# Kernel optimization log

Hardware: AMD Instinct MI355X
Metric: run time of the kernel (lower is better)

## Reference

```python
import jax, jax.numpy as jnp
import numpy as np

NVOC = 50257
DIM = 256
HID = 256
NUM_LAYERS = 2
SEQ = 128
BATCH = 16


def setup_inputs() -> dict:
    key = jax.random.key(0)
    ks = jax.random.split(key, 16)
    u = 0.1
    inp = {
        "tokens": jax.random.randint(ks[0], (SEQ, BATCH), 0, NVOC),
        "emb": jax.random.uniform(ks[1], (NVOC, DIM), jnp.float32, -u, u),
        # gate weights are zero-initialized nn.Parameters in the original; use small
        # random values so gradients/activations are non-degenerate
        "wf": jax.random.normal(ks[2], (HID, HID), jnp.float32) * 0.05,
        "uf": jax.random.normal(ks[3], (DIM, HID), jnp.float32) * 0.05,
        "bf": jnp.zeros((HID,), jnp.float32),
        "wi": jax.random.normal(ks[4], (HID, HID), jnp.float32) * 0.05,
        "ui": jax.random.normal(ks[5], (DIM, HID), jnp.float32) * 0.05,
        "bi": jnp.zeros((HID,), jnp.float32),
        "wc": jax.random.normal(ks[6], (HID, HID), jnp.float32) * 0.05,
        "uc": jax.random.normal(ks[7], (DIM, HID), jnp.float32) * 0.05,
        "bc": jnp.zeros((HID,), jnp.float32),
        "wo": jax.random.normal(ks[8], (HID, HID), jnp.float32) * 0.05,
        "uo": jax.random.normal(ks[9], (DIM, HID), jnp.float32) * 0.05,
        "bo": jnp.zeros((HID,), jnp.float32),
        "dec_w": jax.random.uniform(ks[10], (NVOC, HID), jnp.float32, -u, u),
        "dec_b": jnp.zeros((NVOC,), jnp.float32),
    }
    return inp


def reference(tokens, emb, wf, uf, bf, wi, ui, bi, wc, uc, bc, wo, uo, bo,
              dec_w, dec_b):
    # embeddings: (T, B, D); dropout is identity (eval / p honored as 0)
    x_seq = emb[tokens]

    h0 = jnp.zeros((NUM_LAYERS, BATCH, HID), jnp.float32)
    c0 = jnp.zeros((NUM_LAYERS, BATCH, HID), jnp.float32)

    def step(carry, x_t):
        h, c = carry
        x = x_t  # (B, D)
        hs, cs = [], []
        for l in range(NUM_LAYERS):  # fixed small structural loop
            hp, cp = h[l], c[l]
            f = jax.nn.sigmoid(hp @ wf + x @ uf + bf)
            i = jax.nn.sigmoid(hp @ wi + x @ ui + bi)
            o = jax.nn.sigmoid(hp @ wo + x @ uo + bo)
            g = jnp.tanh(hp @ wc + x @ uc + bc)
            cn = f * cp + i * g
            hn = o * jnp.tanh(cn)
            hs.append(hn)
            cs.append(cn)
            x = hn  # next layer consumes this layer's hidden state
        return (jnp.stack(hs), jnp.stack(cs)), x  # emit top-layer h

    (hT, cT), h_top = jax.lax.scan(step, (h0, c0), x_seq)  # h_top: (T, B, H)
    logits = jnp.einsum('tbh,vh->tbv', h_top, dec_w) + dec_b  # (T, B, V)
    return logits, hT, cT
```

## Files before the change

kernel.cpp:

```cpp
#include <hip/hip_runtime.h>
#include <hip/hip_bf16.h>

#define NVOC 50257
#define DIM 256
#define HID 256
#define NLAYER 2
#define SEQ 128
#define BATCH 16
#define GUARD (1 << 20)
#define NCHUNK 197
#define DECBLKS (32 * NCHUNK)

typedef __bf16 bf16x8 __attribute__((ext_vector_type(8)));
typedef float f32x4 __attribute__((ext_vector_type(4)));
typedef unsigned short u16;
typedef unsigned int u32;
typedef unsigned long long u64;

#define AL64(p)   __hip_atomic_load((const u64*)(p), __ATOMIC_RELAXED, __HIP_MEMORY_SCOPE_AGENT)
#define AS32(p,v) __hip_atomic_store((u32*)(p), (v), __ATOMIC_RELAXED, __HIP_MEMORY_SCOPE_AGENT)

__device__ __forceinline__ float fsig(float z) { return 1.f / (1.f + __expf(-z)); }
__device__ __forceinline__ float ftanh(float z) {
  const float x = fminf(fmaxf(z, -15.f), 15.f);
  const float e = __expf(2.f * x);
  return (e - 1.f) / (e + 1.f);
}
__device__ __forceinline__ bf16x8 cvt8(const float4 u0, const float4 u1) {
  bf16x8 v;
  v[0] = (__bf16)u0.x; v[1] = (__bf16)u0.y; v[2] = (__bf16)u0.z; v[3] = (__bf16)u0.w;
  v[4] = (__bf16)u1.x; v[5] = (__bf16)u1.y; v[6] = (__bf16)u1.z; v[7] = (__bf16)u1.w;
  return v;
}

__global__ void zero_kernel(u32* __restrict__ flg) {
  for (int i = threadIdx.x; i < SEQ * 8; i += 256) AS32(&flg[i], 0u);
}

__global__ __launch_bounds__(256) void xu_kernel(
    const int* __restrict__ tokp, const float* __restrict__ embp,
    const float* __restrict__ uF, const float* __restrict__ uI,
    const float* __restrict__ uC, const float* __restrict__ uO,
    const float* __restrict__ bF, const float* __restrict__ bI,
    const float* __restrict__ bC, const float* __restrict__ bO,
    float* __restrict__ XU)
{
  const int tid = threadIdx.x;
  const int lane = tid & 63, wv = tid >> 6, r16 = lane & 15, kgrp = lane >> 4;
  const int m0 = blockIdx.x * 16;
  const int n0 = blockIdx.y * 256 + wv * 64;
  const float* Ug[4] = {uF, uI, uC, uO};
  const float* Bp[4] = {bF, bI, bC, bO};

  bf16x8 b[4][8];
  float bias[4];
#pragma unroll
  for (int nt = 0; nt < 4; ++nt) {
    const int n = n0 + nt * 16 + r16;
    const float* U = Ug[n >> 8];
    const int c = n & 255;
    bias[nt] = Bp[n >> 8][c];
#pragma unroll
    for (int kk = 0; kk < 8; ++kk) {
      const int kb = kk * 32 + kgrp * 8;
      bf16x8 v;
#pragma unroll
      for (int e = 0; e < 8; ++e) v[e] = (__bf16)U[(size_t)(kb + e) * HID + c];
      b[nt][kk] = v;
    }
  }

  const int tok = tokp[m0 + r16];
  const float* x = embp + (size_t)tok * DIM;
  bf16x8 a[8];
#pragma unroll
  for (int kk = 0; kk < 8; ++kk) {
    const int kb = kk * 32 + kgrp * 8;
    a[kk] = cvt8(*reinterpret_cast<const float4*>(x + kb),
                 *reinterpret_cast<const float4*>(x + kb + 4));
  }
#pragma unroll
  for (int nt = 0; nt < 4; ++nt) {
    f32x4 acc = {0.f, 0.f, 0.f, 0.f};
#pragma unroll
    for (int kk = 0; kk < 8; ++kk)
      acc = __builtin_amdgcn_mfma_f32_16x16x32_bf16(a[kk], b[nt][kk], acc, 0, 0, 0);
    const int n = n0 + nt * 16 + r16;
#pragma unroll
    for (int r = 0; r < 4; ++r)
      XU[(size_t)(m0 + kgrp * 4 + r) * 1024 + n] = acc[r] + bias[nt];
  }
}

__global__ __launch_bounds__(512, 2) void mega_kernel(
    const float* __restrict__ wF, const float* __restrict__ wI,
    const float* __restrict__ wC, const float* __restrict__ wO,
    const float* __restrict__ uF, const float* __restrict__ uI,
    const float* __restrict__ uC, const float* __restrict__ uO,
    const float* __restrict__ bF, const float* __restrict__ bI,
    const float* __restrict__ bC, const float* __restrict__ bO,
    const float* __restrict__ XU, u32* __restrict__ h0w, u32* __restrict__ h1w,
    u32* __restrict__ flg, const float* __restrict__ dw,
    const float* __restrict__ dbp, float* __restrict__ dout)
{
  const int tid  = threadIdx.x;
  const int lane = tid & 63;
  const int wv   = tid >> 6;
  const int r16  = lane & 15;
  const int kgrp = lane >> 4;
  const int bx   = blockIdx.x;

  __shared__ float gbuf[4][16][72];

  if (bx >= 8) {
    const int db = bx - 8;
    const int mb = db / NCHUNK;
    const int nb = db - mb * NCHUNK;
    const int n0 = nb * 256 + wv * 32;

    bf16x8 b[2][8];
    float bb[2];
#pragma unroll
    for (int nt = 0; nt < 2; ++nt) {
      const int v = n0 + nt * 16 + r16;
      const int vc = (v < NVOC) ? v : (NVOC - 1);
      bb[nt] = dbp[vc];
      const float* bp = dw + (size_t)vc * HID + kgrp * 8;
#pragma unroll
      for (int kk = 0; kk < 8; ++kk)
        b[nt][kk] = cvt8(*reinterpret_cast<const float4*>(bp + kk * 32),
                         *reinterpret_cast<const float4*>(bp + kk * 32 + 4));
    }

    if (tid == 0) {
      const int tl = mb * 4 + 3;
      int gd = 0;
      for (;;) {
        const u64 f0 = AL64(flg + (size_t)tl * 8 + 4);
        const u64 f1 = AL64(flg + (size_t)tl * 8 + 6);
        if (((u32)f0 & (u32)(f0 >> 32) & (u32)f1 & (u32)(f1 >> 32)) != 0u) break;
        if (++gd >= GUARD) break;
        __builtin_amdgcn_s_sleep(64);
      }
    }
    __syncthreads();

    const u16* htb = (const u16*)h1w;
    bf16x8 a[4][8];
#pragma unroll
    for (int mt = 0; mt < 4; ++mt) {
      const u16* ap = htb + ((size_t)(mb * 64 + mt * 16 + r16)) * HID + kgrp * 8;
#pragma unroll
      for (int kk = 0; kk < 8; ++kk)
        a[mt][kk] = *reinterpret_cast<const bf16x8*>(ap + kk * 32);
    }

    f32x4 acc[4][2];
#pragma unroll
    for (int mt = 0; mt < 4; ++mt)
#pragma unroll
      for (int nt = 0; nt < 2; ++nt) {
        acc[mt][nt][0] = 0.f; acc[mt][nt][1] = 0.f;
        acc[mt][nt][2] = 0.f; acc[mt][nt][3] = 0.f;
      }
#pragma unroll
    for (int kk = 0; kk < 8; ++kk)
#pragma unroll
      for (int nt = 0; nt < 2; ++nt) {
        const bf16x8 bv = b[nt][kk];
#pragma unroll
        for (int mt = 0; mt < 4; ++mt)
          acc[mt][nt] = __builtin_amdgcn_mfma_f32_16x16x32_bf16(a[mt][kk], bv, acc[mt][nt], 0, 0, 0);
      }

#pragma unroll
    for (int nt = 0; nt < 2; ++nt) {
      const int v = n0 + nt * 16 + r16;
      if (v < NVOC) {
#pragma unroll
        for (int mt = 0; mt < 4; ++mt)
#pragma unroll
          for (int r = 0; r < 4; ++r)
            dout[(size_t)(mb * 64 + mt * 16 + kgrp * 4 + r) * NVOC + v] = acc[mt][nt][r] + bb[nt];
      }
    }
    return;
  }

  const int colt = wv & 3;
  const int gp   = wv >> 2;
  const int l    = bx >> 2;
  const int jj   = bx & 3;
  const int n    = jj * 64 + colt * 16 + r16;
  const int g0   = gp * 2;

  const float* Wg[4] = {wF, wI, wC, wO};
  const float* Ug[4] = {uF, uI, uC, uO};
  const float* Bg[4] = {bF, bI, bC, bO};
  const u16* h0s = (const u16*)h0w;
  const u16* h1s = (const u16*)h1w;
  const size_t logitsN = (size_t)SEQ * BATCH * NVOC;

  bf16x8 wa[2][8];
  bf16x8 wb[2][8];
  float bias[2];
#pragma unroll
  for (int gi = 0; gi < 2; ++gi) {
    const int g = g0 + gi;
    bias[gi] = Bg[g][n];
#pragma unroll
    for (int kk = 0; kk < 8; ++kk) {
      const int kb = kk * 32 + kgrp * 8;
      bf16x8 v;
#pragma unroll
      for (int e = 0; e < 8; ++e) v[e] = (__bf16)Wg[g][(size_t)(kb + e) * HID + n];
      wa[gi][kk] = v;
      if (l == 1) {
        bf16x8 u;
#pragma unroll
        for (int e = 0; e < 8; ++e) u[e] = (__bf16)Ug[g][(size_t)(kb + e) * HID + n];
        wb[gi][kk] = u;
      }
    }
  }

  const int eb = tid >> 5;
  const int ec = (tid & 31) * 2;
  float c0 = 0.f, c1 = 0.f;

  for (int t = 0; t < SEQ; ++t) {
    f32x4 acc[2];
#pragma unroll
    for (int gi = 0; gi < 2; ++gi) { acc[gi][0]=0.f; acc[gi][1]=0.f; acc[gi][2]=0.f; acc[gi][3]=0.f; }

    float xuv[2][4];
    if (l == 0) {
#pragma unroll
      for (int gi = 0; gi < 2; ++gi)
#pragma unroll
        for (int r = 0; r < 4; ++r)
          xuv[gi][r] = XU[(size_t)(t * 16 + kgrp * 4 + r) * 1024 + (g0 + gi) * 256 + n];

      if (t > 0) {
        if (tid == 0) {
          int gd = 0;
          for (;;) {
            const u64 f0 = AL64(flg + (size_t)(t - 1) * 8);
            const u64 f1 = AL64(flg + (size_t)(t - 1) * 8 + 2);
            if (((u32)f0 & (u32)(f0 >> 32) & (u32)f1 & (u32)(f1 >> 32)) != 0u) break;
            if (++gd >= GUARD) break;
          }
        }
        __syncthreads();
        const u16* hp = h0s + ((size_t)(t - 1) * BATCH + r16) * HID + kgrp * 8;
        bf16x8 hA[8];
#pragma unroll
        for (int kk = 0; kk < 8; ++kk)
          hA[kk] = *reinterpret_cast<const bf16x8*>(hp + kk * 32);
#pragma unroll
        for (int kk = 0; kk < 8; ++kk)
#pragma unroll
          for (int gi = 0; gi < 2; ++gi)
            acc[gi] = __builtin_amdgcn_mfma_f32_16x16x32_bf16(hA[kk], wa[gi][kk], acc[gi], 0, 0, 0);
      }
    } else {
      if (t > 0) {
        if (tid == 0) {
          int gd = 0;
          for (;;) {
            const u64 g1 = AL64(flg + (size_t)(t - 1) * 8 + 4);
            const u64 g2 = AL64(flg + (size_t)(t - 1) * 8 + 6);
            if (((u32)g1 & (u32)(g1 >> 32) & (u32)g2 & (u32)(g2 >> 32)) != 0u) break;
            if (++gd >= GUARD) break;
          }
        }
        __syncthreads();
        const u16* hp = h1s + ((size_t)(t - 1) * BATCH + r16) * HID + kgrp * 8;
        bf16x8 hB[8];
#pragma unroll
        for (int kk = 0; kk < 8; ++kk)
          hB[kk] = *reinterpret_cast<const bf16x8*>(hp + kk * 32);
#pragma unroll
        for (int kk = 0; kk < 8; ++kk)
#pragma unroll
          for (int gi = 0; gi < 2; ++gi)
            acc[gi] = __builtin_amdgcn_mfma_f32_16x16x32_bf16(hB[kk], wa[gi][kk], acc[gi], 0, 0, 0);
      }
      if (tid == 0) {
        int gd = 0;
        for (;;) {
          const u64 f0 = AL64(flg + (size_t)t * 8);
          const u64 f1 = AL64(flg + (size_t)t * 8 + 2);
          if (((u32)f0 & (u32)(f0 >> 32) & (u32)f1 & (u32)(f1 >> 32)) != 0u) break;
          if (++gd >= GUARD) break;
        }
      }
      __syncthreads();
      const u16* xp = h0s + ((size_t)t * BATCH + r16) * HID + kgrp * 8;
      bf16x8 hA[8];
#pragma unroll
      for (int kk = 0; kk < 8; ++kk)
        hA[kk] = *reinterpret_cast<const bf16x8*>(xp + kk * 32);
#pragma unroll
      for (int kk = 0; kk < 8; ++kk)
#pragma unroll
        for (int gi = 0; gi < 2; ++gi)
          acc[gi] = __builtin_amdgcn_mfma_f32_16x16x32_bf16(hA[kk], wb[gi][kk], acc[gi], 0, 0, 0);
    }

#pragma unroll
    for (int gi = 0; gi < 2; ++gi) {
      const int g = g0 + gi;
#pragma unroll
      for (int r = 0; r < 4; ++r) {
        const float z = acc[gi][r] + ((l == 0) ? xuv[gi][r] : bias[gi]);
        gbuf[g][kgrp * 4 + r][colt * 16 + r16] = (g == 2) ? ftanh(z) : fsig(z);
      }
    }
    __syncthreads();

    const float ff0 = gbuf[0][eb][ec], ff1 = gbuf[0][eb][ec + 1];
    const float ii0 = gbuf[1][eb][ec], ii1 = gbuf[1][eb][ec + 1];
    const float gg0 = gbuf[2][eb][ec], gg1 = gbuf[2][eb][ec + 1];
    const float oo0 = gbuf[3][eb][ec], oo1 = gbuf[3][eb][ec + 1];
    c0 = ff0 * c0 + ii0 * gg0;
    c1 = ff1 * c1 + ii1 * gg1;
    const float hv0 = oo0 * ftanh(c0);
    const float hv1 = oo1 * ftanh(c1);
    const u32 pk = (u32)__builtin_bit_cast(u16, (__bf16)hv0) |
                   ((u32)__builtin_bit_cast(u16, (__bf16)hv1) << 16);
    u32* hw = l ? h1w : h0w;
    AS32(hw + ((size_t)t * BATCH + eb) * 128 + jj * 32 + (ec >> 1), pk);

    if (t == SEQ - 1) {
      const int nn = jj * 64 + ec;
      float* hT = dout + logitsN + ((size_t)l * BATCH + eb) * HID + nn;
      float* cT = dout + logitsN + (size_t)NLAYER * BATCH * HID + ((size_t)l * BATCH + eb) * HID + nn;
      hT[0] = hv0; hT[1] = hv1;
      cT[0] = c0;  cT[1] = c1;
    }
    __syncthreads();
    if (tid == 0) AS32(&flg[(size_t)t * 8 + l * 4 + jj], 1u);
  }
}

extern "C" void kernel_launch(void* const* d_in, const int* in_sizes, int n_in,
                              void* d_out, int out_size, void* d_ws, size_t ws_size,
                              hipStream_t stream) {
  const int*   tokp = (const int*)d_in[0];
  const float* embp = (const float*)d_in[1];
  const float* wF = (const float*)d_in[2];
  const float* uF = (const float*)d_in[3];
  const float* bF = (const float*)d_in[4];
  const float* wI = (const float*)d_in[5];
  const float* uI = (const float*)d_in[6];
  const float* bI = (const float*)d_in[7];
  const float* wC = (const float*)d_in[8];
  const float* uC = (const float*)d_in[9];
  const float* bC = (const float*)d_in[10];
  const float* wO = (const float*)d_in[11];
  const float* uO = (const float*)d_in[12];
  const float* bO = (const float*)d_in[13];
  const float* dw = (const float*)d_in[14];
  const float* db = (const float*)d_in[15];
  float* out = (float*)d_out;

  char* ws = (char*)d_ws;
  size_t off = 0;
  float* XU = (float*)(ws + off); off += (size_t)SEQ * BATCH * 1024 * 4;
  u32* h0w = (u32*)(ws + off); off += (size_t)SEQ * BATCH * HID * 2;
  u32* h1w = (u32*)(ws + off); off += (size_t)SEQ * BATCH * HID * 2;
  u32* flg = (u32*)(ws + off); off += (size_t)SEQ * 8 * 4;

  zero_kernel<<<1, 256, 0, stream>>>(flg);
  xu_kernel<<<dim3(128, 4), 256, 0, stream>>>(tokp, embp, uF, uI, uC, uO,
                                              bF, bI, bC, bO, XU);
  mega_kernel<<<8 + DECBLKS, 512, 0, stream>>>(wF, wI, wC, wO, uF, uI, uC, uO,
                                               bF, bI, bC, bO, XU, h0w, h1w, flg,
                                               dw, db, out);
}
```

Before: 857.0 us.

## Split recurrent LSTM into per-wave layer roles with a separate layer-1 input-projection stage

The recurrent part is restructured into three roles of 2 blocks each: layer-0 recurrence, a layer-1 input projection (h0 @ U) that writes to a new V buffer, and layer-1 recurrence. Each wave now owns 16 columns across all four gates, so the LDS gate exchange and block-wide __syncthreads are removed. Per-wave flags (16 per role per step) are used instead of per-block flags. This takes the layer-1 input matmul off the layer-1 critical path and makes synchronisation finer-grained. In exchange it adds a global round-trip through V, more flag polling traffic, and a lower occupancy hint (launch_bounds 512,1).

```diff
diff --git a/kernel.cpp b/kernel.cpp
--- a/kernel.cpp
+++ b/kernel.cpp
@@ -10,6 +10,10 @@
 #define GUARD (1 << 20)
 #define NCHUNK 197
 #define DECBLKS (32 * NCHUNK)
+#define FL_L0 0
+#define FL_XV 16
+#define FL_L1 32
+#define FSTR 64
 
 typedef __bf16 bf16x8 __attribute__((ext_vector_type(8)));
 typedef float f32x4 __attribute__((ext_vector_type(4)));
@@ -33,8 +37,21 @@
   return v;
 }
 
+__device__ __forceinline__ bool all16(const u32* fp) {
+  const u64 m = AL64(fp) & AL64(fp + 2) & AL64(fp + 4) & AL64(fp + 6)
+              & AL64(fp + 8) & AL64(fp + 10) & AL64(fp + 12) & AL64(fp + 14);
+  return ((u32)m & (u32)(m >> 32)) != 0u;
+}
+__device__ __forceinline__ void pollwave(const u32* fp, int lane) {
+  if (lane == 0) {
+    int gd = 0;
+    while (!all16(fp) && ++gd < GUARD) {}
+  }
+  asm volatile("" ::: "memory");
+}
+
 __global__ void zero_kernel(u32* __restrict__ flg) {
-  for (int i = threadIdx.x; i < SEQ * 8; i += 256) AS32(&flg[i], 0u);
+  for (int i = threadIdx.x; i < SEQ * FSTR; i += 256) AS32(&flg[i], 0u);
 }
 
 __global__ __launch_bounds__(256) void xu_kernel(
@@ -92,14 +109,15 @@
   }
 }
 
-__global__ __launch_bounds__(512, 2) void mega_kernel(
+__global__ __launch_bounds__(512, 1) void mega_kernel(
     const float* __restrict__ wF, const float* __restrict__ wI,
     const float* __restrict__ wC, const float* __restrict__ wO,
     const float* __restrict__ uF, const float* __restrict__ uI,
     const float* __restrict__ uC, const float* __restrict__ uO,
     const float* __restrict__ bF, const float* __restrict__ bI,
     const float* __restrict__ bC, const float* __restrict__ bO,
-    const float* __restrict__ XU, u32* __restrict__ h0w, u32* __restrict__ h1w,
+    const float* __restrict__ XU, float* __restrict__ V,
+    u32* __restrict__ h0w, u32* __restrict__ h1w,
     u32* __restrict__ flg, const float* __restrict__ dw,
     const float* __restrict__ dbp, float* __restrict__ dout)
 {
@@ -110,10 +128,8 @@
   const int kgrp = lane >> 4;
   const int bx   = blockIdx.x;
 
-  __shared__ float gbuf[4][16][72];
-
-  if (bx >= 8) {
-    const int db = bx - 8;
+  if (bx >= 6) {
+    const int db = bx - 6;
     const int mb = db / NCHUNK;
     const int nb = db - mb * NCHUNK;
     const int n0 = nb * 256 + wv * 32;
@@ -133,15 +149,9 @@
     }
 
     if (tid == 0) {
-      const int tl = mb * 4 + 3;
+      const u32* fp = flg + (size_t)(mb * 4 + 3) * FSTR + FL_L1;
       int gd = 0;
-      for (;;) {
-        const u64 f0 = AL64(flg + (size_t)tl * 8 + 4);
-        const u64 f1 = AL64(flg + (size_t)tl * 8 + 6);
-        if (((u32)f0 & (u32)(f0 >> 32) & (u32)f1 & (u32)(f1 >> 32)) != 0u) break;
-        if (++gd >= GUARD) break;
-        __builtin_amdgcn_s_sleep(64);
-      }
+      while (!all16(fp) && ++gd < GUARD) __builtin_amdgcn_s_sleep(64);
     }
     __syncthreads();
 
@@ -187,160 +197,149 @@
     return;
   }
 
-  const int colt = wv & 3;
-  const int gp   = wv >> 2;
-  const int l    = bx >> 2;
-  const int jj   = bx & 3;
-  const int n    = jj * 64 + colt * 16 + r16;
-  const int g0   = gp * 2;
-
+  const int role = bx >> 1;
+  const int wk   = (bx & 1) * 8 + wv;
   const float* Wg[4] = {wF, wI, wC, wO};
   const float* Ug[4] = {uF, uI, uC, uO};
   const float* Bg[4] = {bF, bI, bC, bO};
   const u16* h0s = (const u16*)h0w;
   const u16* h1s = (const u16*)h1w;
   const size_t logitsN = (size_t)SEQ * BATCH * NVOC;
-
-  bf16x8 wa[2][8];
-  bf16x8 wb[2][8];
-  float bias[2];
-#pragma unroll
-  for (int gi = 0; gi < 2; ++gi) {
-    const int g = g0 + gi;
-    bias[gi] = Bg[g][n];
+  const int odd = lane & 1;
+
+  if (role == 1) {
+    bf16x8 u[4][8];
+    float bias[4];
+#pragma unroll
+    for (int nt = 0; nt < 4; ++nt) {
+      const int gcol = wk * 64 + nt * 16 + r16;
+      const float* U = Ug[gcol >> 8];
+      const int c = gcol & 255;
+      bias[nt] = Bg[gcol >> 8][c];
+#pragma unroll
+      for (int kk = 0; kk < 8; ++kk) {
+        const int kb = kk * 32 + kgrp * 8;
+        bf16x8 v;
+#pragma unroll
+        for (int e = 0; e < 8; ++e) v[e] = (__bf16)U[(size_t)(kb + e) * HID + c];
+        u[nt][kk] = v;
+      }
+    }
+
+    for (int t = 0; t < SEQ; ++t) {
+      pollwave(flg + (size_t)t * FSTR + FL_L0, lane);
+      const u16* hp = h0s + ((size_t)t * BATCH + r16) * HID + kgrp * 8;
+      bf16x8 hA[8];
+#pragma unroll
+      for (int kk = 0; kk < 8; ++kk)
+        hA[kk] = *reinterpret_cast<const bf16x8*>(hp + kk * 32);
+
+      f32x4 acc[4];
+#pragma unroll
+      for (int nt = 0; nt < 4; ++nt) { acc[nt][0]=0.f; acc[nt][1]=0.f; acc[nt][2]=0.f; acc[nt][3]=0.f; }
+#pragma unroll
+      for (int kk = 0; kk < 8; ++kk)
+#pragma unroll
+        for (int nt = 0; nt < 4; ++nt)
+          acc[nt] = __builtin_amdgcn_mfma_f32_16x16x32_bf16(hA[kk], u[nt][kk], acc[nt], 0, 0, 0);
+
+#pragma unroll
+      for (int nt = 0; nt < 4; ++nt) {
+        const int gcol = wk * 64 + nt * 16 + r16;
+#pragma unroll
+        for (int r = 0; r < 4; ++r)
+          AS32((u32*)(V + ((size_t)(t * 16 + kgrp * 4 + r)) * 1024 + gcol),
+               __builtin_bit_cast(u32, acc[nt][r] + bias[nt]));
+      }
+      asm volatile("s_waitcnt vmcnt(0)" ::: "memory");
+      if (lane == 0) AS32(&flg[(size_t)t * FSTR + FL_XV + wk], 1u);
+    }
+    return;
+  }
+
+  const int col = wk * 16 + r16;
+  bf16x8 wa[4][8];
+#pragma unroll
+  for (int g = 0; g < 4; ++g)
 #pragma unroll
     for (int kk = 0; kk < 8; ++kk) {
       const int kb = kk * 32 + kgrp * 8;
       bf16x8 v;
 #pragma unroll
-      for (int e = 0; e < 8; ++e) v[e] = (__bf16)Wg[g][(size_t)(kb + e) * HID + n];
-      wa[gi][kk] = v;
-      if (l == 1) {
-        bf16x8 u;
-#pragma unroll
-        for (int e = 0; e < 8; ++e) u[e] = (__bf16)Ug[g][(size_t)(kb + e) * HID + n];
-        wb[gi][kk] = u;
-      }
-    }
-  }
-
-  const int eb = tid >> 5;
-  const int ec = (tid & 31) * 2;
-  float c0 = 0.f, c1 = 0.f;
+      for (int e = 0; e < 8; ++e) v[e] = (__bf16)Wg[g][(size_t)(kb + e) * HID + col];
+      wa[g][kk] = v;
+    }
+
+  float cst[4] = {0.f, 0.f, 0.f, 0.f};
+  u32* hw = (role == 0) ? h0w : h1w;
+  const u16* hs = (role == 0) ? h0s : h1s;
+  const int flbase = (role == 0) ? FL_L0 : FL_L1;
 
   for (int t = 0; t < SEQ; ++t) {
-    f32x4 acc[2];
-#pragma unroll
-    for (int gi = 0; gi < 2; ++gi) { acc[gi][0]=0.f; acc[gi][1]=0.f; acc[gi][2]=0.f; acc[gi][3]=0.f; }
-
-    float xuv[2][4];
-    if (l == 0) {
-#pragma unroll
-      for (int gi = 0; gi < 2; ++gi)
+    f32x4 acc[4];
+#pragma unroll
+    for (int g = 0; g < 4; ++g) { acc[g][0]=0.f; acc[g][1]=0.f; acc[g][2]=0.f; acc[g][3]=0.f; }
+
+    if (t > 0) {
+      pollwave(flg + (size_t)(t - 1) * FSTR + flbase, lane);
+      const u16* hp = hs + ((size_t)(t - 1) * BATCH + r16) * HID + kgrp * 8;
+      bf16x8 hA[8];
+#pragma unroll
+      for (int kk = 0; kk < 8; ++kk)
+        hA[kk] = *reinterpret_cast<const bf16x8*>(hp + kk * 32);
+#pragma unroll
+      for (int kk = 0; kk < 8; ++kk)
+#pragma unroll
+        for (int g = 0; g < 4; ++g)
+          acc[g] = __builtin_amdgcn_mfma_f32_16x16x32_bf16(hA[kk], wa[g][kk], acc[g], 0, 0, 0);
+    }
+
+    float xin[4][4];
+    if (role == 0) {
+#pragma unroll
+      for (int g = 0; g < 4; ++g)
 #pragma unroll
         for (int r = 0; r < 4; ++r)
-          xuv[gi][r] = XU[(size_t)(t * 16 + kgrp * 4 + r) * 1024 + (g0 + gi) * 256 + n];
-
-      if (t > 0) {
-        if (tid == 0) {
-          int gd = 0;
-          for (;;) {
-            const u64 f0 = AL64(flg + (size_t)(t - 1) * 8);
-            const u64 f1 = AL64(flg + (size_t)(t - 1) * 8 + 2);
-            if (((u32)f0 & (u32)(f0 >> 32) & (u32)f1 & (u32)(f1 >> 32)) != 0u) break;
-            if (++gd >= GUARD) break;
-          }
-        }
-        __syncthreads();
-        const u16* hp = h0s + ((size_t)(t - 1) * BATCH + r16) * HID + kgrp * 8;
-        bf16x8 hA[8];
-#pragma unroll
-        for (int kk = 0; kk < 8; ++kk)
-          hA[kk] = *reinterpret_cast<const bf16x8*>(hp + kk * 32);
-#pragma unroll
-        for (int kk = 0; kk < 8; ++kk)
-#pragma unroll
-          for (int gi = 0; gi < 2; ++gi)
-            acc[gi] = __builtin_amdgcn_mfma_f32_16x16x32_bf16(hA[kk], wa[gi][kk], acc[gi], 0, 0, 0);
-      }
+          xin[g][r] = XU[(size_t)(t * 16 + kgrp * 4 + r) * 1024 + g * 256 + col];
     } else {
-      if (t > 0) {
-        if (tid == 0) {
-          int gd = 0;
-          for (;;) {
-            const u64 g1 = AL64(flg + (size_t)(t - 1) * 8 + 4);
-            const u64 g2 = AL64(flg + (size_t)(t - 1) * 8 + 6);
-            if (((u32)g1 & (u32)(g1 >> 32) & (u32)g2 & (u32)(g2 >> 32)) != 0u) break;
-            if (++gd >= GUARD) break;
-          }
-        }
-        __syncthreads();
-        const u16* hp = h1s + ((size_t)(t - 1) * BATCH + r16) * HID + kgrp * 8;
-        bf16x8 hB[8];
-#pragma unroll
-        for (int kk = 0; kk < 8; ++kk)
-          hB[kk] = *reinterpret_cast<const bf16x8*>(hp + kk * 32);
-#pragma unroll
-        for (int kk = 0; kk < 8; ++kk)
-#pragma unroll
-          for (int gi = 0; gi < 2; ++gi)
-            acc[gi] = __builtin_amdgcn_mfma_f32_16x16x32_bf16(hB[kk], wa[gi][kk], acc[gi], 0, 0, 0);
-      }
-      if (tid == 0) {
-        int gd = 0;
-        for (;;) {
-          const u64 f0 = AL64(flg + (size_t)t * 8);
-          const u64 f1 = AL64(flg + (size_t)t * 8 + 2);
-          if (((u32)f0 & (u32)(f0 >> 32) & (u32)f1 & (u32)(f1 >> 32)) != 0u) break;
-          if (++gd >= GUARD) break;
-        }
-      }
-      __syncthreads();
-      const u16* xp = h0s + ((size_t)t * BATCH + r16) * HID + kgrp * 8;
-      bf16x8 hA[8];
-#pragma unroll
-      for (int kk = 0; kk < 8; ++kk)
-        hA[kk] = *reinterpret_cast<const bf16x8*>(xp + kk * 32);
-#pragma unroll
-      for (int kk = 0; kk < 8; ++kk)
-#pragma unroll
-        for (int gi = 0; gi < 2; ++gi)
-          acc[gi] = __builtin_amdgcn_mfma_f32_16x16x32_bf16(hA[kk], wb[gi][kk], acc[gi], 0, 0, 0);
-    }
-
-#pragma unroll
-    for (int gi = 0; gi < 2; ++gi) {
-      const int g = g0 + gi;
+      pollwave(flg + (size_t)t * FSTR + FL_XV, lane);
+#pragma unroll
+      for (int g = 0; g < 4; ++g)
+#pragma unroll
+        for (int r = 0; r < 4; ++r)
+          xin[g][r] = V[(size_t)(t * 16 + kgrp * 4 + r) * 1024 + g * 256 + col];
+    }
+
+    float hv[4];
+#pragma unroll
+    for (int r = 0; r < 4; ++r) {
+      const float f = fsig(acc[0][r] + xin[0][r]);
+      const float i = fsig(acc[1][r] + xin[1][r]);
+      const float g = ftanh(acc[2][r] + xin[2][r]);
+      const float o = fsig(acc[3][r] + xin[3][r]);
+      cst[r] = f * cst[r] + i * g;
+      hv[r] = o * ftanh(cst[r]);
+    }
+#pragma unroll
+    for (int r = 0; r < 4; ++r) {
+      const float ph = __shfl_xor(hv[r], 1);
+      const u16 a = __builtin_bit_cast(u16, (__bf16)hv[r]);
+      const u16 p = __builtin_bit_cast(u16, (__bf16)ph);
+      const u32 pk = odd ? ((u32)p | ((u32)a << 16)) : ((u32)a | ((u32)p << 16));
+      if ((r & 1) == odd)
+        AS32(hw + ((size_t)t * BATCH + kgrp * 4 + r) * 128 + (col >> 1), pk);
+    }
+    if (t == SEQ - 1) {
+      const int lb = (role == 0) ? 0 : BATCH;
 #pragma unroll
       for (int r = 0; r < 4; ++r) {
-        const float z = acc[gi][r] + ((l == 0) ? xuv[gi][r] : bias[gi]);
-        gbuf[g][kgrp * 4 + r][colt * 16 + r16] = (g == 2) ? ftanh(z) : fsig(z);
-      }
-    }
-    __syncthreads();
-
-    const float ff0 = gbuf[0][eb][ec], ff1 = gbuf[0][eb][ec + 1];
-    const float ii0 = gbuf[1][eb][ec], ii1 = gbuf[1][eb][ec + 1];
-    const float gg0 = gbuf[2][eb][ec], gg1 = gbuf[2][eb][ec + 1];
-    const float oo0 = gbuf[3][eb][ec], oo1 = gbuf[3][eb][ec + 1];
-    c0 = ff0 * c0 + ii0 * gg0;
-    c1 = ff1 * c1 + ii1 * gg1;
-    const float hv0 = oo0 * ftanh(c0);
-    const float hv1 = oo1 * ftanh(c1);
-    const u32 pk = (u32)__builtin_bit_cast(u16, (__bf16)hv0) |
-                   ((u32)__builtin_bit_cast(u16, (__bf16)hv1) << 16);
-    u32* hw = l ? h1w : h0w;
-    AS32(hw + ((size_t)t * BATCH + eb) * 128 + jj * 32 + (ec >> 1), pk);
-
-    if (t == SEQ - 1) {
-      const int nn = jj * 64 + ec;
-      float* hT = dout + logitsN + ((size_t)l * BATCH + eb) * HID + nn;
-      float* cT = dout + logitsN + (size_t)NLAYER * BATCH * HID + ((size_t)l * BATCH + eb) * HID + nn;
-      hT[0] = hv0; hT[1] = hv1;
-      cT[0] = c0;  cT[1] = c1;
-    }
-    __syncthreads();
-    if (tid == 0) AS32(&flg[(size_t)t * 8 + l * 4 + jj], 1u);
+        const int b = kgrp * 4 + r;
+        dout[logitsN + (size_t)(lb + b) * HID + col] = hv[r];
+        dout[logitsN + (size_t)NLAYER * BATCH * HID + (size_t)(lb + b) * HID + col] = cst[r];
+      }
+    }
+    asm volatile("s_waitcnt vmcnt(0)" ::: "memory");
+    if (lane == 0) AS32(&flg[(size_t)t * FSTR + flbase + wk], 1u);
   }
 }
 
@@ -368,14 +367,15 @@
   char* ws = (char*)d_ws;
   size_t off = 0;
   float* XU = (float*)(ws + off); off += (size_t)SEQ * BATCH * 1024 * 4;
+  float* V  = (float*)(ws + off); off += (size_t)SEQ * BATCH * 1024 * 4;
   u32* h0w = (u32*)(ws + off); off += (size_t)SEQ * BATCH * HID * 2;
   u32* h1w = (u32*)(ws + off); off += (size_t)SEQ * BATCH * HID * 2;
-  u32* flg = (u32*)(ws + off); off += (size_t)SEQ * 8 * 4;
+  u32* flg = (u32*)(ws + off); off += (size_t)SEQ * FSTR * 4;
 
   zero_kernel<<<1, 256, 0, stream>>>(flg);
   xu_kernel<<<dim3(128, 4), 256, 0, stream>>>(tokp, embp, uF, uI, uC, uO,
                                               bF, bI, bC, bO, XU);
-  mega_kernel<<<8 + DECBLKS, 512, 0, stream>>>(wF, wI, wC, wO, uF, uI, uC, uO,
-                                               bF, bI, bC, bO, XU, h0w, h1w, flg,
-                                               dw, db, out);
-}
+  mega_kernel<<<6 + DECBLKS, 512, 0, stream>>>(wF, wI, wC, wO, uF, uI, uC, uO,
+                                               bF, bI, bC, bO, XU, V, h0w, h1w,
+                                               flg, dw, db, out);
+}
```

Measured after the change: 1.028 ms. +19.9%, slower.
